# Performance work log

Measured on AMD Instinct MI355X. Metric: run time of the kernel, lower is better.

The kernel has to match this reference:

```python
import jax, jax.numpy as jnp
import numpy as np

S, B, H = 2048, 2, 2048
NH = 16
HD = H // NH  # 128
ROPE_BASE = 10000.0


def _rope_cos_sin(seq_len, dim, dtype):
    inv_freq = 1.0 / (ROPE_BASE ** (jnp.arange(0, dim, 2, dtype=jnp.float32) / dim))
    t = jnp.arange(seq_len, dtype=jnp.float32)
    freqs = jnp.outer(t, inv_freq)            # [S, dim/2]
    emb = jnp.concatenate([freqs, freqs], -1)  # [S, dim]
    return jnp.cos(emb).astype(dtype), jnp.sin(emb).astype(dtype)


def _rotate_half(x):
    x1, x2 = jnp.split(x, 2, axis=-1)
    return jnp.concatenate([-x2, x1], axis=-1)


def setup_inputs() -> dict:
    key = jax.random.key(0)
    k1, k2, k3 = jax.random.split(key, 3)
    hidden_states = jax.random.normal(k1, (S, B, H), dtype=jnp.float32)
    w_qkv = jax.random.normal(k2, (3 * H, H), dtype=jnp.float32) * (1.0 / np.sqrt(H))
    w_out = jax.random.normal(k3, (H, H), dtype=jnp.float32) * (1.0 / np.sqrt(H))
    return {"hidden_states": hidden_states, "w_qkv": w_qkv, "w_out": w_out}


def reference(hidden_states, w_qkv, w_out):
    seq_len, batch, _ = hidden_states.shape
    # QKV projection (nn.Linear: x @ W^T), bias=False
    qkv = jnp.einsum('sbh,oh->sbo', hidden_states, w_qkv)
    qkv = qkv.reshape(seq_len, batch, 3, NH, HD)
    q, k, v = qkv[:, :, 0], qkv[:, :, 1], qkv[:, :, 2]  # [S, B, NH, HD]

    cos, sin = _rope_cos_sin(seq_len, HD, hidden_states.dtype)
    cos = cos[:, None, None, :]
    sin = sin[:, None, None, :]
    q = q * cos + _rotate_half(q) * sin
    k = k * cos + _rotate_half(k) * sin

    # [S, B, NH, HD] -> [B, NH, S, HD]
    q = q.transpose(1, 2, 0, 3)
    k = k.transpose(1, 2, 0, 3)
    v = v.transpose(1, 2, 0, 3)

    scale = 1.0 / np.sqrt(HD)
    scores = jnp.einsum('bhqd,bhkd->bhqk', q, k) * scale
    causal = jnp.tril(jnp.ones((seq_len, seq_len), dtype=bool))
    scores = jnp.where(causal, scores, jnp.finfo(scores.dtype).min)
    probs = jax.nn.softmax(scores, axis=-1)
    attn = jnp.einsum('bhqk,bhkd->bhqd', probs, v)  # [B, NH, S, HD]

    # [B, NH, S, HD] -> [S, B, NH*HD]
    out = attn.transpose(2, 0, 1, 3).reshape(seq_len, batch, -1)
    out = jnp.einsum('sbh,oh->sbo', out, w_out)
    return out
```

## Files before the change

kernel.cpp:

```cpp
#include <hip/hip_runtime.h>
#include <hip/hip_bf16.h>

typedef __attribute__((ext_vector_type(8))) short bf16x8;
typedef __attribute__((ext_vector_type(8))) short s16x8;
typedef __attribute__((ext_vector_type(4))) float f32x4;
typedef __attribute__((ext_vector_type(4))) int i32x4;

#define SEQ 2048
#define BATCH 2
#define HID 2048
#define NH 16
#define HD 128
#define QKVN 6144

static __device__ __forceinline__ short f2bf(float f) {
    union { float f; unsigned u; } v; v.f = f;
    unsigned r = (v.u + 0x7FFFu + ((v.u >> 16) & 1u)) >> 16;
    return (short)r;
}

static __device__ __forceinline__ void gload_lds16(const short* g, short* l) {
    __builtin_amdgcn_global_load_lds((const __attribute__((address_space(1))) void*)g,
                                     (__attribute__((address_space(3))) void*)l, 16, 0, 0);
}

static __device__ __forceinline__ void cvt_body(const float* in, short* out, int i) {
    f32x4 a = *(const f32x4*)(in + (size_t)i * 8);
    f32x4 b = *(const f32x4*)(in + (size_t)i * 8 + 4);
    s16x8 o = { f2bf(a.x), f2bf(a.y), f2bf(a.z), f2bf(a.w),
                f2bf(b.x), f2bf(b.y), f2bf(b.z), f2bf(b.w) };
    *(s16x8*)(out + (size_t)i * 8) = o;
}

__global__ void cvt_kernel(const float* __restrict__ in, short* __restrict__ out, int n8) {
    const int i = blockIdx.x * 256 + threadIdx.x;
    if (i >= n8) return;
    cvt_body(in, out, i);
}

__global__ void cvt2_kernel(const float* __restrict__ inA, short* __restrict__ outA,
                            const float* __restrict__ inB, short* __restrict__ outB) {
    const int bid = blockIdx.x;
    if (bid < 4096) cvt_body(inA, outA, bid * 256 + threadIdx.x);
    else            cvt_body(inB, outB, (bid - 4096) * 256 + threadIdx.x);
}

#define G128_STAGE_A(BUF, HA, KK) do { \
    const short* _s = ((HA) ? aS1 : aS0) + (size_t)(KK) * 64; \
    short* _d = lds + (BUF) * 16384 + (HA) * 8192 + w * 512; \
    gload_lds16(_s, _d); \
    gload_lds16(_s + (size_t)128 * K, _d + 4096); \
} while (0)

#define G128_STAGE_B(BUF, HB, KK) do { \
    const short* _s = ((HB) ? bS1 : bS0) + (size_t)(KK) * 64; \
    short* _d = lds + 32768 + (BUF) * 8192 + (HB) * 4096 + w * 512; \
    gload_lds16(_s, _d); \
} while (0)

#define G128_LOAD_A(HA) do { \
    const short* _p = lds + bufR * 16384 + (HA) * 8192; \
    _Pragma("unroll") \
    for (int mm = 0; mm < 2; ++mm) { \
        aR[mm][0] = *(const bf16x8*)(_p + aOff0 + mm * 1024); \
        aR[mm][1] = *(const bf16x8*)(_p + aOff1 + mm * 1024); \
    } \
} while (0)

#define G128_LOAD_B(HB) do { \
    const short* _p = lds + 32768 + bufR * 8192 + (HB) * 4096; \
    _Pragma("unroll") \
    for (int nn = 0; nn < 2; ++nn) { \
        bR[(HB) * 2 + nn][0] = *(const bf16x8*)(_p + bOff0 + nn * 2048); \
        bR[(HB) * 2 + nn][1] = *(const bf16x8*)(_p + bOff1 + nn * 2048); \
    } \
} while (0)

#define G128_MFMA(HA, HB) do { \
    _Pragma("unroll") \
    for (int mm = 0; mm < 2; ++mm) { \
        _Pragma("unroll") \
        for (int nn = 0; nn < 2; ++nn) { \
            f32x4 _c = acc[(HA) * 2 + mm][(HB) * 2 + nn]; \
            _c = __builtin_amdgcn_mfma_f32_16x16x32_bf16(aR[mm][0], bR[(HB) * 2 + nn][0], _c, 0, 0, 0); \
            _c = __builtin_amdgcn_mfma_f32_16x16x32_bf16(aR[mm][1], bR[(HB) * 2 + nn][1], _c, 0, 0, 0); \
            acc[(HA) * 2 + mm][(HB) * 2 + nn] = _c; \
        } \
    } \
} while (0)

template<int MODE>
__global__ __launch_bounds__(512, 2)
void gemm128n(const short* __restrict__ A, const short* __restrict__ B,
              void* __restrict__ Cp, int N, int K) {
    __shared__ short lds[49152];

    const int tid = threadIdx.x;
    const int mBase = blockIdx.y * 256;
    const int nBase = blockIdx.x * 128;
    const int w = tid >> 6, lane = tid & 63, quad = lane >> 4, l15 = lane & 15;
    const int wm = w >> 1, wn = w & 1;

    const int kcol = 8 * ((tid & 7) ^ ((tid >> 3) & 7));
    const int srow = ((tid >> 3) & 15) + (tid >> 7) * 32;
    const short* aS0 = A + (size_t)(mBase + srow) * K + kcol;
    const short* aS1 = aS0 + (size_t)16 * K;
    const short* bS0 = B + (size_t)(nBase + srow) * K + kcol;
    const short* bS1 = bS0 + (size_t)16 * K;

    const int cs0 = (quad * 8) ^ ((l15 & 7) << 3);
    const int aOff0 = (l15 + wm * 32) * 64 + cs0;
    const int aOff1 = aOff0 ^ 32;
    const int bOff0 = (l15 + wn * 16) * 64 + cs0;
    const int bOff1 = bOff0 ^ 32;

    const int NK = K >> 6;
    f32x4 acc[4][4] = {};
    bf16x8 aR[2][2], bR[4][2];

    G128_STAGE_A(0, 0, 0); G128_STAGE_B(0, 0, 0); G128_STAGE_B(0, 1, 0); G128_STAGE_A(0, 1, 0);
    G128_STAGE_A(1, 0, 1); G128_STAGE_B(1, 0, 1); G128_STAGE_B(1, 1, 1);
    asm volatile("s_waitcnt vmcnt(4)" ::: "memory");
    __builtin_amdgcn_s_barrier();

    int bufR = 0;
    for (int k = 0; k < NK; ++k) {
        const int kk1 = (k + 1 < NK) ? k + 1 : NK - 1;
        const int kk2 = (k + 2 < NK) ? k + 2 : NK - 1;
        G128_LOAD_A(0);
        G128_LOAD_B(0);
        G128_STAGE_A(bufR ^ 1, 1, kk1);
        asm volatile("s_waitcnt lgkmcnt(4)" ::: "memory");
        __builtin_amdgcn_s_barrier();
        asm volatile("s_waitcnt lgkmcnt(0)" ::: "memory");
        __builtin_amdgcn_s_setprio(1);
        G128_MFMA(0, 0);
        __builtin_amdgcn_s_setprio(0);
        __builtin_amdgcn_s_barrier();
        G128_LOAD_B(1);
        G128_STAGE_A(bufR, 0, kk2);
        __builtin_amdgcn_s_barrier();
        asm volatile("s_waitcnt lgkmcnt(0)" ::: "memory");
        __builtin_amdgcn_s_setprio(1);
        G128_MFMA(0, 1);
        __builtin_amdgcn_s_setprio(0);
        __builtin_amdgcn_s_barrier();
        G128_LOAD_A(1);
        G128_STAGE_B(bufR, 0, kk2);
        __builtin_amdgcn_s_barrier();
        asm volatile("s_waitcnt lgkmcnt(0)" ::: "memory");
        __builtin_amdgcn_s_setprio(1);
        G128_MFMA(1, 1);
        __builtin_amdgcn_s_setprio(0);
        __builtin_amdgcn_s_barrier();
        G128_STAGE_B(bufR, 1, kk2);
        asm volatile("s_waitcnt vmcnt(4)" ::: "memory");
        __builtin_amdgcn_s_barrier();
        __builtin_amdgcn_s_setprio(1);
        G128_MFMA(1, 0);
        __builtin_amdgcn_s_setprio(0);
        __builtin_amdgcn_s_barrier();
        bufR ^= 1;
    }
    asm volatile("s_waitcnt vmcnt(0)" ::: "memory");

    if (MODE == 1 && nBase < 4096) {
        const float post = (nBase < 2048) ? 0.08838834764831845f : 1.0f;
        short* C = (short*)Cp;
        #pragma unroll
        for (int af = 0; af < 4; ++af) {
            const int ha = af >> 1, mm = af & 1;
            const int row0 = mBase + wm * 64 + (2 * mm + ha) * 16 + quad * 4;
            #pragma unroll
            for (int hb = 0; hb < 2; ++hb) {
                const int d = wn * 32 + hb * 16 + l15;
                const float inv_freq =
                    expf(-((float)(2 * d) * (1.0f / 128.0f)) * 9.210340371976184f);
                #pragma unroll
                for (int rp = 0; rp < 2; ++rp) {
                    const int s = (row0 >> 1) + rp;
                    float sn, cs;
                    sincosf((float)s * inv_freq, &sn, &cs);
                    #pragma unroll
                    for (int rr = 0; rr < 2; ++rr) {
                        const int r = rp * 2 + rr;
                        const float x1 = acc[af][hb * 2 + 0][r];
                        const float x2 = acc[af][hb * 2 + 1][r];
                        const size_t rb = (size_t)(row0 + r) * N + nBase + d;
                        C[rb]      = f2bf((x1 * cs - x2 * sn) * post);
                        C[rb + 64] = f2bf((x2 * cs + x1 * sn) * post);
                    }
                }
            }
        }
    } else {
        #pragma unroll
        for (int af = 0; af < 4; ++af) {
            const int ha = af >> 1, mm = af & 1;
            const int row0 = mBase + wm * 64 + (2 * mm + ha) * 16 + quad * 4;
            #pragma unroll
            for (int bg = 0; bg < 4; ++bg) {
                const int hb = bg >> 1, nn = bg & 1;
                const int col = nBase + nn * 64 + wn * 32 + hb * 16 + l15;
                #pragma unroll
                for (int r = 0; r < 4; ++r) {
                    if (MODE == 1)
                        ((short*)Cp)[(size_t)(row0 + r) * N + col] = f2bf(acc[af][bg][r]);
                    else
                        ((float*)Cp)[(size_t)(row0 + r) * N + col] = acc[af][bg][r];
                }
            }
        }
    }
}

__global__ void vtrans_kernel(const short* __restrict__ qkv, short* __restrict__ vT) {
    __shared__ short T[64][72];
    const int s0 = blockIdx.x * 64, d0 = blockIdx.y * 64;
    const int bh = blockIdx.z;
    const int b = bh >> 4, h = bh & 15;
    const int t = threadIdx.x;

    #pragma unroll
    for (int p = 0; p < 2; ++p) {
        const int sl = (t >> 3) + p * 32;
        const int dl = (t & 7) * 8;
        *(i32x4*)&T[sl][dl] =
            *(const i32x4*)(qkv + (size_t)((s0 + sl) * 2 + b) * QKVN + 4096 + h * 128 + d0 + dl);
    }
    __syncthreads();
    #pragma unroll
    for (int p = 0; p < 2; ++p) {
        const int dl = (t >> 3) + p * 32;
        const int sl = (t & 7) * 8;
        short tmp[8];
        #pragma unroll
        for (int j = 0; j < 8; ++j) tmp[j] = T[sl + j][dl];
        *(i32x4*)(vT + ((size_t)bh * 128 + d0 + dl) * 2048 + s0 + sl) = *(i32x4*)tmp;
    }
}

__global__ __launch_bounds__(256, 2)
void attn_kernel(const short* __restrict__ qkv, const short* __restrict__ vT,
                 short* __restrict__ out) {
    __shared__ short lds[40960];

    const int bx = blockIdx.x;
    const int h = blockIdx.y, b = blockIdx.z;
    const int Aq = (bx & 1) ? (bx >> 1) : (15 - (bx >> 1));
    const int qt = b ? (15 - Aq) : Aq;
    const int tid = threadIdx.x;
    const int w = tid >> 6, lane = tid & 63, quad = lane >> 4, l15 = lane & 15;
    const int bh = b * 16 + h;
    const int cswz = (l15 & 7) << 3;

    bf16x8 aq[2][4];
    #pragma unroll
    for (int m = 0; m < 2; ++m) {
        const short* qbase =
            qkv + (size_t)((qt * 128 + w * 32 + m * 16 + l15) * 2 + b) * QKVN + h * 128;
        #pragma unroll
        for (int c = 0; c < 4; ++c)
            aq[m][c] = *(const bf16x8*)(qbase + c * 32 + quad * 8);
    }

    f32x4 oacc[2][8] = {};
    float lpart[2][4] = {};

    const short* kSrc0 = qkv + (size_t)((w * 16 + (lane >> 4)) * 2 + b) * QKVN
                       + 2048 + h * 128 + ((lane & 15) ^ (lane >> 4)) * 8;
    const short* kSrc1 = qkv + (size_t)((w * 16 + 4 + (lane >> 4)) * 2 + b) * QKVN
                       + 2048 + h * 128 + ((lane & 15) ^ (4 | (lane >> 4))) * 8;
    const short* vSrc = vT + ((size_t)bh * 128 + w * 32 + (lane >> 3)) * 2048
                      + ((lane & 7) ^ ((lane >> 3) & 7)) * 8;
    short* kDst = lds + w * 2048;
    short* vDst = lds + 16384 + w * 2048;

#define STAGE_KV(BUF, KK0) do { \
    const size_t kAdv = (size_t)(KK0) * 2 * QKVN; \
    short* _kd = kDst + (BUF) * 8192; \
    short* _vd = vDst + (BUF) * 8192; \
    gload_lds16(kSrc0 + kAdv,                  _kd); \
    gload_lds16(kSrc1 + kAdv,                  _kd + 512); \
    gload_lds16(kSrc0 + kAdv + 16 * QKVN,      _kd + 1024); \
    gload_lds16(kSrc1 + kAdv + 16 * QKVN,      _kd + 1536); \
    gload_lds16(vSrc + (KK0),                  _vd); \
    gload_lds16(vSrc + (KK0) + 8 * 2048,       _vd + 512); \
    gload_lds16(vSrc + (KK0) + 16 * 2048,      _vd + 1024); \
    gload_lds16(vSrc + (KK0) + 24 * 2048,      _vd + 1536); \
} while (0)

    const int nChunks = 2 * qt + 2;

    STAGE_KV(0, 0);
    asm volatile("s_waitcnt vmcnt(0)" ::: "memory");
    __builtin_amdgcn_s_barrier();

    for (int ck = 0; ck < nChunks; ++ck) {
        const int cur = ck & 1;
        const int kk0 = ck * 64;
        if (ck + 1 < nChunks) STAGE_KV(cur ^ 1, kk0 + 64);

        const short* Kc = lds + cur * 8192;
        const short* Vc = lds + 16384 + cur * 8192;
        short* Pw = lds + 32768 + w * 2048;

        f32x4 sc4[2][4] = {};
        #pragma unroll
        for (int c = 0; c < 4; ++c) {
            const int cb = (c * 32 + quad * 8) ^ cswz;
            #pragma unroll
            for (int n = 0; n < 4; ++n) {
                bf16x8 bk = *(const bf16x8*)(Kc + (n * 16 + l15) * 128 + cb);
                sc4[0][n] = __builtin_amdgcn_mfma_f32_16x16x32_bf16(aq[0][c], bk, sc4[0][n], 0, 0, 0);
                sc4[1][n] = __builtin_amdgcn_mfma_f32_16x16x32_bf16(aq[1][c], bk, sc4[1][n], 0, 0, 0);
            }
        }

        const bool diag = (ck >= 2 * qt);
        #pragma unroll
        for (int m = 0; m < 2; ++m) {
            const int rowbase = qt * 128 + w * 32 + m * 16 + quad * 4;
            #pragma unroll
            for (int r = 0; r < 4; ++r) {
                const int prow = m * 16 + quad * 4 + r;
                const int pswz = ((quad * 4 + r) & 7) << 3;
                #pragma unroll
                for (int n = 0; n < 4; ++n) {
                    float sv = sc4[m][n][r];
                    if (diag && (kk0 + n * 16 + l15 > rowbase + r)) sv = -1e30f;
                    const float p = __expf(sv);
                    lpart[m][r] += p;
                    Pw[prow * 64 + ((n * 16 + l15) ^ pswz)] = f2bf(p);
                }
            }
        }

        #pragma unroll
        for (int kp2 = 0; kp2 < 2; ++kp2) {
            const int cb = (kp2 * 32 + quad * 8) ^ cswz;
            bf16x8 ap0 = *(const bf16x8*)(Pw + l15 * 64 + cb);
            bf16x8 ap1 = *(const bf16x8*)(Pw + (16 + l15) * 64 + cb);
            #pragma unroll
            for (int dt = 0; dt < 8; ++dt) {
                bf16x8 bv = *(const bf16x8*)(Vc + (dt * 16 + l15) * 64 + cb);
                oacc[0][dt] = __builtin_amdgcn_mfma_f32_16x16x32_bf16(ap0, bv, oacc[0][dt], 0, 0, 0);
                oacc[1][dt] = __builtin_amdgcn_mfma_f32_16x16x32_bf16(ap1, bv, oacc[1][dt], 0, 0, 0);
            }
        }

        asm volatile("s_waitcnt vmcnt(0)" ::: "memory");
        __builtin_amdgcn_s_barrier();
    }
#undef STAGE_KV

    #pragma unroll
    for (int m = 0; m < 2; ++m) {
        const int rowbase = qt * 128 + w * 32 + m * 16 + quad * 4;
        #pragma unroll
        for (int r = 0; r < 4; ++r) {
            float l = lpart[m][r];
            #pragma unroll
            for (int off = 1; off < 16; off <<= 1)
                l += __shfl_xor(l, off);
            const float inv_l = 1.0f / l;
            const size_t obase = (size_t)((rowbase + r) * 2 + b) * HID + h * 128;
            #pragma unroll
            for (int dt = 0; dt < 8; ++dt)
                out[obase + dt * 16 + l15] = f2bf(oacc[m][dt][r] * inv_l);
        }
    }
}

extern "C" void kernel_launch(void* const* d_in, const int* in_sizes, int n_in,
                              void* d_out, int out_size, void* d_ws, size_t ws_size,
                              hipStream_t stream) {
    const float* hidden = (const float*)d_in[0];
    const float* w_qkv  = (const float*)d_in[1];
    const float* w_out  = (const float*)d_in[2];
    float* out = (float*)d_out;

    short* qkv     = (short*)d_ws;
    short* attnb   = qkv + (size_t)4096 * QKVN;
    short* wqkv_bf = attnb + (size_t)4096 * HID;
    short* wout_bf = wqkv_bf;
    short* hbf     = wqkv_bf + (size_t)QKVN * HID;
    short* vT      = hbf;

    dim3 blk(256);
    cvt2_kernel<<<dim3(4096 + 6144), blk, 0, stream>>>(hidden, hbf, w_qkv, wqkv_bf);
    gemm128n<1><<<dim3(QKVN / 128, 4096 / 256), dim3(512), 0, stream>>>(
        hbf, wqkv_bf, qkv, QKVN, HID);
    cvt_kernel<<<dim3(2048), blk, 0, stream>>>(w_out, wout_bf, 2048 * 256);
    vtrans_kernel<<<dim3(SEQ / 64, HD / 64, BATCH * NH), blk, 0, stream>>>(qkv, vT);
    attn_kernel<<<dim3(SEQ / 128, NH, BATCH), blk, 0, stream>>>(qkv, vT, attnb);
    gemm128n<0><<<dim3(HID / 128, 4096 / 256), dim3(512), 0, stream>>>(
        attnb, wout_bf, out, HID, HID);
}
```

Baseline: 346.4 us.

## Fuse V transpose into QKV GEMM epilogue and use fast RoPE intrinsics

Result: no change. 345.8 us (-0.2%).

```diff
diff --git a/kernel.cpp b/kernel.cpp
--- a/kernel.cpp
+++ b/kernel.cpp
@@ -5,6 +5,7 @@
 typedef __attribute__((ext_vector_type(8))) short s16x8;
 typedef __attribute__((ext_vector_type(4))) float f32x4;
 typedef __attribute__((ext_vector_type(4))) int i32x4;
+typedef __attribute__((ext_vector_type(2))) unsigned u32x2;
 
 #define SEQ 2048
 #define BATCH 2
@@ -12,6 +13,7 @@
 #define NH 16
 #define HD 128
 #define QKVN 6144
+#define QKN 4096
 
 static __device__ __forceinline__ short f2bf(float f) {
     union { float f; unsigned u; } v; v.f = f;
@@ -92,7 +94,7 @@
 template<int MODE>
 __global__ __launch_bounds__(512, 2)
 void gemm128n(const short* __restrict__ A, const short* __restrict__ B,
-              void* __restrict__ Cp, int N, int K) {
+              void* __restrict__ Cp, short* __restrict__ vTp, int N, int K) {
     __shared__ short lds[49152];
 
     const int tid = threadIdx.x;
@@ -175,24 +177,54 @@
             for (int hb = 0; hb < 2; ++hb) {
                 const int d = wn * 32 + hb * 16 + l15;
                 const float inv_freq =
-                    expf(-((float)(2 * d) * (1.0f / 128.0f)) * 9.210340371976184f);
+                    __expf(-((float)(2 * d) * (1.0f / 128.0f)) * 9.210340371976184f);
                 #pragma unroll
                 for (int rp = 0; rp < 2; ++rp) {
                     const int s = (row0 >> 1) + rp;
                     float sn, cs;
-                    sincosf((float)s * inv_freq, &sn, &cs);
+                    __sincosf((float)s * inv_freq, &sn, &cs);
                     #pragma unroll
                     for (int rr = 0; rr < 2; ++rr) {
                         const int r = rp * 2 + rr;
                         const float x1 = acc[af][hb * 2 + 0][r];
                         const float x2 = acc[af][hb * 2 + 1][r];
-                        const size_t rb = (size_t)(row0 + r) * N + nBase + d;
+                        const size_t rb = (size_t)(row0 + r) * QKN + nBase + d;
                         C[rb]      = f2bf((x1 * cs - x2 * sn) * post);
                         C[rb + 64] = f2bf((x2 * cs + x1 * sn) * post);
                     }
                 }
             }
         }
+    } else if (MODE == 1) {
+        __builtin_amdgcn_s_barrier();
+        #pragma unroll
+        for (int af = 0; af < 4; ++af) {
+            const int ha = af >> 1, mm = af & 1;
+            const int rbase = wm * 64 + (2 * mm + ha) * 16 + quad * 4;
+            #pragma unroll
+            for (int bg = 0; bg < 4; ++bg) {
+                const int hb = bg >> 1, nn = bg & 1;
+                const int d = nn * 64 + wn * 32 + hb * 16 + l15;
+                #pragma unroll
+                for (int bb = 0; bb < 2; ++bb) {
+                    const unsigned lo = (unsigned short)f2bf(acc[af][bg][bb]);
+                    const unsigned hi = (unsigned short)f2bf(acc[af][bg][bb + 2]);
+                    *(unsigned*)&lds[bb * 16896 + d * 132 + (rbase >> 1)] =
+                        lo | (hi << 16);
+                }
+            }
+        }
+        __syncthreads();
+        const int h = (nBase - 4096) >> 7;
+        const int s0 = mBase >> 1;
+        const int hw = tid >> 5, l5 = tid & 31;
+        #pragma unroll
+        for (int pass = 0; pass < 16; ++pass) {
+            const int rho = pass * 16 + hw;
+            const int bb = rho >> 7, dd = rho & 127;
+            const u32x2 v2 = *(const u32x2*)&lds[bb * 16896 + dd * 132 + l5 * 4];
+            *(u32x2*)&vTp[((size_t)(bb * 16 + h) * 128 + dd) * 2048 + s0 + l5 * 4] = v2;
+        }
     } else {
         #pragma unroll
         for (int af = 0; af < 4; ++af) {
@@ -203,40 +235,10 @@
                 const int hb = bg >> 1, nn = bg & 1;
                 const int col = nBase + nn * 64 + wn * 32 + hb * 16 + l15;
                 #pragma unroll
-                for (int r = 0; r < 4; ++r) {
-                    if (MODE == 1)
-                        ((short*)Cp)[(size_t)(row0 + r) * N + col] = f2bf(acc[af][bg][r]);
-                    else
-                        ((float*)Cp)[(size_t)(row0 + r) * N + col] = acc[af][bg][r];
-                }
-            }
-        }
-    }
-}
-
-__global__ void vtrans_kernel(const short* __restrict__ qkv, short* __restrict__ vT) {
-    __shared__ short T[64][72];
-    const int s0 = blockIdx.x * 64, d0 = blockIdx.y * 64;
-    const int bh = blockIdx.z;
-    const int b = bh >> 4, h = bh & 15;
-    const int t = threadIdx.x;
-
-    #pragma unroll
-    for (int p = 0; p < 2; ++p) {
-        const int sl = (t >> 3) + p * 32;
-        const int dl = (t & 7) * 8;
-        *(i32x4*)&T[sl][dl] =
-            *(const i32x4*)(qkv + (size_t)((s0 + sl) * 2 + b) * QKVN + 4096 + h * 128 + d0 + dl);
-    }
-    __syncthreads();
-    #pragma unroll
-    for (int p = 0; p < 2; ++p) {
-        const int dl = (t >> 3) + p * 32;
-        const int sl = (t & 7) * 8;
-        short tmp[8];
-        #pragma unroll
-        for (int j = 0; j < 8; ++j) tmp[j] = T[sl + j][dl];
-        *(i32x4*)(vT + ((size_t)bh * 128 + d0 + dl) * 2048 + s0 + sl) = *(i32x4*)tmp;
+                for (int r = 0; r < 4; ++r)
+                    ((float*)Cp)[(size_t)(row0 + r) * N + col] = acc[af][bg][r];
+            }
+        }
     }
 }
 
@@ -258,7 +260,7 @@
     #pragma unroll
     for (int m = 0; m < 2; ++m) {
         const short* qbase =
-            qkv + (size_t)((qt * 128 + w * 32 + m * 16 + l15) * 2 + b) * QKVN + h * 128;
+            qkv + (size_t)((qt * 128 + w * 32 + m * 16 + l15) * 2 + b) * QKN + h * 128;
         #pragma unroll
         for (int c = 0; c < 4; ++c)
             aq[m][c] = *(const bf16x8*)(qbase + c * 32 + quad * 8);
@@ -267,9 +269,9 @@
     f32x4 oacc[2][8] = {};
     float lpart[2][4] = {};
 
-    const short* kSrc0 = qkv + (size_t)((w * 16 + (lane >> 4)) * 2 + b) * QKVN
+    const short* kSrc0 = qkv + (size_t)((w * 16 + (lane >> 4)) * 2 + b) * QKN
                        + 2048 + h * 128 + ((lane & 15) ^ (lane >> 4)) * 8;
-    const short* kSrc1 = qkv + (size_t)((w * 16 + 4 + (lane >> 4)) * 2 + b) * QKVN
+    const short* kSrc1 = qkv + (size_t)((w * 16 + 4 + (lane >> 4)) * 2 + b) * QKN
                        + 2048 + h * 128 + ((lane & 15) ^ (4 | (lane >> 4))) * 8;
     const short* vSrc = vT + ((size_t)bh * 128 + w * 32 + (lane >> 3)) * 2048
                       + ((lane & 7) ^ ((lane >> 3) & 7)) * 8;
@@ -277,13 +279,13 @@
     short* vDst = lds + 16384 + w * 2048;
 
 #define STAGE_KV(BUF, KK0) do { \
-    const size_t kAdv = (size_t)(KK0) * 2 * QKVN; \
+    const size_t kAdv = (size_t)(KK0) * 2 * QKN; \
     short* _kd = kDst + (BUF) * 8192; \
     short* _vd = vDst + (BUF) * 8192; \
     gload_lds16(kSrc0 + kAdv,                  _kd); \
     gload_lds16(kSrc1 + kAdv,                  _kd + 512); \
-    gload_lds16(kSrc0 + kAdv + 16 * QKVN,      _kd + 1024); \
-    gload_lds16(kSrc1 + kAdv + 16 * QKVN,      _kd + 1536); \
+    gload_lds16(kSrc0 + kAdv + 16 * QKN,       _kd + 1024); \
+    gload_lds16(kSrc1 + kAdv + 16 * QKN,       _kd + 1536); \
     gload_lds16(vSrc + (KK0),                  _vd); \
     gload_lds16(vSrc + (KK0) + 8 * 2048,       _vd + 512); \
     gload_lds16(vSrc + (KK0) + 16 * 2048,      _vd + 1024); \
@@ -381,19 +383,18 @@
     float* out = (float*)d_out;
 
     short* qkv     = (short*)d_ws;
-    short* attnb   = qkv + (size_t)4096 * QKVN;
+    short* attnb   = qkv + (size_t)4096 * QKN;
     short* wqkv_bf = attnb + (size_t)4096 * HID;
     short* wout_bf = wqkv_bf;
     short* hbf     = wqkv_bf + (size_t)QKVN * HID;
-    short* vT      = hbf;
+    short* vT      = hbf + (size_t)4096 * HID;
 
     dim3 blk(256);
     cvt2_kernel<<<dim3(4096 + 6144), blk, 0, stream>>>(hidden, hbf, w_qkv, wqkv_bf);
     gemm128n<1><<<dim3(QKVN / 128, 4096 / 256), dim3(512), 0, stream>>>(
-        hbf, wqkv_bf, qkv, QKVN, HID);
+        hbf, wqkv_bf, qkv, vT, QKVN, HID);
     cvt_kernel<<<dim3(2048), blk, 0, stream>>>(w_out, wout_bf, 2048 * 256);
-    vtrans_kernel<<<dim3(SEQ / 64, HD / 64, BATCH * NH), blk, 0, stream>>>(qkv, vT);
     attn_kernel<<<dim3(SEQ / 128, NH, BATCH), blk, 0, stream>>>(qkv, vT, attnb);
     gemm128n<0><<<dim3(HID / 128, 4096 / 256), dim3(512), 0, stream>>>(
-        attnb, wout_bf, out, HID, HID);
-}
+        attnb, wout_bf, out, nullptr, HID, HID);
+}
```
